# Optimization experiments

Measured on AMD Instinct MI355X. Metric: run time of the kernel, lower is better.

Reference implementation:

```python
import jax, jax.numpy as jnp
import numpy as np

B, F, H, OUT, S = 32768, 256, 128, 64, 6
RELAX, EPS, BN_EPS = 1.5, 1e-05, 1e-05
SQRT_HALF = 0.7071067811865476


def _bn(h, g, b):
    # training-mode BatchNorm1d: biased batch statistics over dim 0
    m = h.mean(axis=0)
    v = h.var(axis=0)
    return (h - m) * jax.lax.rsqrt(v + BN_EPS) * g + b


def _tfrm(x, W, g, b, glu_act=True):
    h = _bn(x @ W, g, b)
    if glu_act:
        d = h.shape[1] // 2
        h = h[:, :d] * jax.nn.sigmoid(h[:, d:])
    return h


def setup_inputs() -> dict:
    key = jax.random.key(0)
    ks = jax.random.split(key, 6)
    f32 = jnp.float32
    return {
        "x": jax.random.normal(ks[0], (B, F), f32),
        "enc_g": jnp.ones((F,), f32), "enc_b": jnp.zeros((F,), f32),
        "W1": jax.random.normal(ks[1], (F, 2 * H), f32) * 0.05,
        "g1": jnp.ones((2 * H,), f32), "b1": jnp.zeros((2 * H,), f32),
        "W2": jax.random.normal(ks[2], (H, 2 * H), f32) * 0.05,
        "g2": jnp.ones((2 * H,), f32), "b2": jnp.zeros((2 * H,), f32),
        "W3": jax.random.normal(ks[3], (S, H, 2 * H), f32) * 0.05,
        "g3": jnp.ones((S, 2 * H), f32), "b3": jnp.zeros((S, 2 * H), f32),
        "W4": jax.random.normal(ks[4], (S, H, 2 * H), f32) * 0.05,
        "g4": jnp.ones((S, 2 * H), f32), "b4": jnp.zeros((S, 2 * H), f32),
        "Wc": jax.random.normal(ks[5], (S - 1, OUT, F), f32) * 0.05,
        "gc": jnp.ones((S - 1, F), f32), "bc": jnp.zeros((S - 1, F), f32),
    }


def reference(x, enc_g, enc_b, W1, g1, b1, W2, g2, b2, W3, g3, b3,
              W4, g4, b4, Wc, gc, bc):
    x = _bn(x, enc_g, enc_b)                      # [B, F]
    masked = x
    compl = jnp.ones((x.shape[0], F), x.dtype)    # complementary aggregated mask
    agg_out, agg_entropy = [], []
    for ni in range(S):
        h = _tfrm(masked, W1, g1, b1)                             # [B, H]
        h = (_tfrm(h, W2, g2, b2) + h) * SQRT_HALF
        h = (_tfrm(h, W3[ni], g3[ni], b3[ni]) + h) * SQRT_HALF
        h = (_tfrm(h, W4[ni], g4[ni], b4[ni]) + h) * SQRT_HALF
        if ni > 0:
            # NOTE: source uses x (not h) here -- replicated faithfully
            agg_out.append(jax.nn.relu(x[:, :OUT]))
        fc = h[:, OUT:]                                           # [B, OUT]
        if ni < S - 1:
            coef = _tfrm(fc, Wc[ni], gc[ni], bc[ni], glu_act=False)  # [B, F]
            mask_values = jax.nn.softmax(coef * compl, axis=1)
            compl = compl * (RELAX - mask_values)
            agg_entropy.append(
                jnp.mean(jnp.sum(-mask_values * jnp.log(mask_values + EPS), axis=1))
                / (S - 1))
            masked = mask_values * x
    out = jnp.sum(jnp.stack(agg_out, axis=0), axis=0)   # [B, OUT]
    entropy = jnp.sum(jnp.stack(agg_entropy))           # scalar
    return (out, entropy)
```

## Files before the change

kernel.cpp:

```cpp
#include <hip/hip_runtime.h>
#include <math.h>

#define BSZ   32768
#define FDIM  256
#define HDIM  128
#define OUTD  64
#define SQRT_HALF 0.70710678118654752f
#define BN_EPS 1e-5f
#define SM_EPS 1e-5f
#define INV_B (1.0f / 32768.0f)
#define NCPY  8
#define SLOT  (NCPY * 512)

typedef __attribute__((ext_vector_type(8))) short bf16x8;
typedef __attribute__((ext_vector_type(4))) float f32x4;

__device__ __forceinline__ float b2f(unsigned short u) {
    return __uint_as_float(((unsigned int)u) << 16);
}
__device__ __forceinline__ unsigned short f2b(float f) {
    unsigned int u = __float_as_uint(f);
    u += 0x7fff + ((u >> 16) & 1);
    return (unsigned short)(u >> 16);
}

__device__ __forceinline__ void async16(const void* g, void* l) {
    __builtin_amdgcn_global_load_lds(
        (const __attribute__((address_space(1))) void*)(uintptr_t)g,
        (__attribute__((address_space(3))) void*)(unsigned int)(uintptr_t)l,
        16, 0, 0);
}

__device__ inline float waveMaxAll(float v) {
#pragma unroll
    for (int m = 32; m > 0; m >>= 1) v = fmaxf(v, __shfl_xor(v, m, 64));
    return v;
}
__device__ inline float waveSumAll(float v) {
#pragma unroll
    for (int m = 32; m > 0; m >>= 1) v += __shfl_xor(v, m, 64);
    return v;
}

__global__ __launch_bounds__(256) void prep_w(
    const float* __restrict__ W1, const float* __restrict__ W2,
    const float* __restrict__ W3, const float* __restrict__ W4,
    const float* __restrict__ Wc,
    unsigned short* __restrict__ W1t, unsigned short* __restrict__ W2t,
    unsigned short* __restrict__ W3t, unsigned short* __restrict__ W4t,
    unsigned short* __restrict__ Wct)
{
    const int m = blockIdx.x, kz = blockIdx.y, n = threadIdx.x;
    const float* src; unsigned short* dst; int K;
    if (m == 0)      { src = W1;                        dst = W1t;               K = 256; }
    else if (m == 1) { src = W2;                        dst = W2t;               K = 128; }
    else if (m < 7)  { int i = m - 2;  src = W3 + (size_t)i * 128 * 256; dst = W3t + (size_t)i * 32768; K = 128; }
    else if (m < 12) { int i = m - 7;  src = W4 + (size_t)i * 128 * 256; dst = W4t + (size_t)i * 32768; K = 128; }
    else             { int i = m - 12; src = Wc + (size_t)i * 64 * 256;  dst = Wct + (size_t)i * 16384; K = 64; }
    const int k0 = kz * 32;
    if (k0 >= K) return;
    for (int k = k0; k < k0 + 32; ++k)
        dst[(size_t)n * K + k] = f2b(src[(size_t)k * 256 + n]);
}

__global__ __launch_bounds__(256) void colstats(const float* __restrict__ X,
                                                float* __restrict__ st0) {
    __shared__ float red[4][512];
    const int sub = threadIdx.x >> 6;
    const int c4  = (threadIdx.x & 63) << 2;
    float s[4] = {0.f, 0.f, 0.f, 0.f}, q[4] = {0.f, 0.f, 0.f, 0.f};
#pragma unroll 8
    for (int i = 0; i < 32; ++i) {
        const int row = blockIdx.x * 128 + i * 4 + sub;
        float4 v = *(const float4*)(X + (size_t)row * 256 + c4);
        s[0] += v.x; q[0] += v.x * v.x;
        s[1] += v.y; q[1] += v.y * v.y;
        s[2] += v.z; q[2] += v.z * v.z;
        s[3] += v.w; q[3] += v.w * v.w;
    }
#pragma unroll
    for (int e = 0; e < 4; ++e) {
        red[sub][c4 + e] = s[e];
        red[sub][256 + c4 + e] = q[e];
    }
    __syncthreads();
    const int t = threadIdx.x;
    const int cp = (blockIdx.x & (NCPY - 1)) * 512;
    float sS = red[0][t] + red[1][t] + red[2][t] + red[3][t];
    float sQ = red[0][256 + t] + red[1][256 + t] + red[2][256 + t] + red[3][256 + t];
    atomicAdd(&st0[cp + t], sS);
    atomicAdd(&st0[cp + 256 + t], sQ);
}

__global__ __launch_bounds__(256) void norm_x(const float* __restrict__ x,
                                              const float* __restrict__ st0,
                                              const float* __restrict__ g,
                                              const float* __restrict__ b,
                                              unsigned short* __restrict__ xb,
                                              float* __restrict__ out) {
    const int i4 = blockIdx.x * 256 + threadIdx.x;
    const int row = i4 >> 6, c4 = (i4 & 63) << 2;
    float4 xv = *(const float4*)(x + (size_t)row * 256 + c4);
    float sS[4] = {0.f, 0.f, 0.f, 0.f}, sQ[4] = {0.f, 0.f, 0.f, 0.f};
#pragma unroll
    for (int cp = 0; cp < NCPY; ++cp) {
        float4 a = *(const float4*)&st0[cp * 512 + c4];
        float4 q = *(const float4*)&st0[cp * 512 + 256 + c4];
        sS[0] += a.x; sS[1] += a.y; sS[2] += a.z; sS[3] += a.w;
        sQ[0] += q.x; sQ[1] += q.y; sQ[2] += q.z; sQ[3] += q.w;
    }
    float4 gv = *(const float4*)&g[c4];
    float4 bv = *(const float4*)&b[c4];
    const float* xp = (const float*)&xv;
    const float* gp = (const float*)&gv; const float* bp = (const float*)&bv;
    float n[4];
    ushort4 ob;
    unsigned short* obp = (unsigned short*)&ob;
#pragma unroll
    for (int e = 0; e < 4; ++e) {
        float mean = sS[e] * INV_B;
        float var  = sQ[e] * INV_B - mean * mean;
        float sc   = gp[e] * rsqrtf(var + BN_EPS);
        float sh   = bp[e] - mean * sc;
        n[e] = xp[e] * sc + sh;
        obp[e] = f2b(n[e]);
    }
    *(ushort4*)(xb + (size_t)row * 256 + c4) = ob;
    if (c4 < OUTD) {
        float4 ov = make_float4(5.0f * fmaxf(n[0], 0.f), 5.0f * fmaxf(n[1], 0.f),
                                5.0f * fmaxf(n[2], 0.f), 5.0f * fmaxf(n[3], 0.f));
        *(float4*)(out + (size_t)row * OUTD + c4) = ov;
    }
}

__device__ __forceinline__ void gemm_epilogue(
    f32x4 (&acc)[4][4], int row0, int wave, int lane, int tid, int bcp,
    float* redS, float* redQ,
    unsigned short* __restrict__ Pout, float* __restrict__ statsOut)
{
    const int fm = lane & 15;
    const int orow = row0 + (lane >> 4) * 4;
    const int ocol = wave * 64 + fm;
#pragma unroll
    for (int i = 0; i < 4; ++i)
#pragma unroll
        for (int j = 0; j < 4; ++j)
#pragma unroll
            for (int r = 0; r < 4; ++r)
                Pout[(size_t)(orow + i * 16 + r) * 256 + (ocol + j * 16)] = f2b(acc[i][j][r]);

#pragma unroll
    for (int j = 0; j < 4; ++j) {
        float s = 0.f, q = 0.f;
#pragma unroll
        for (int i = 0; i < 4; ++i)
#pragma unroll
            for (int r = 0; r < 4; ++r) {
                float v = acc[i][j][r];
                s += v; q += v * v;
            }
        s += __shfl_xor(s, 16, 64); s += __shfl_xor(s, 32, 64);
        q += __shfl_xor(q, 16, 64); q += __shfl_xor(q, 32, 64);
        if (lane < 16) {
            redS[wave * 64 + j * 16 + lane] = s;
            redQ[wave * 64 + j * 16 + lane] = q;
        }
    }
    __syncthreads();
    atomicAdd(&statsOut[bcp + tid], redS[tid]);
    atomicAdd(&statsOut[bcp + 256 + tid], redQ[tid]);
}

__global__ __launch_bounds__(256) void gemm_bf16(
    const unsigned short* __restrict__ A,
    const unsigned short* __restrict__ Wt, int K,
    unsigned short* __restrict__ P,
    float* __restrict__ statsOut)
{
    __shared__ short As[64 * 32];
    __shared__ short Bs[256 * 32];
    __shared__ float redS[256], redQ[256];

    const int tid  = threadIdx.x;
    const int wave = tid >> 6;
    const int lane = tid & 63;
    const int row0 = blockIdx.x * 64;
    const int bcp  = (blockIdx.x & (NCPY - 1)) * 512;

    const int sr = lane >> 2;
    const int sc = (lane & 3) * 8;
    const int fm = lane & 15;
    const int fq = (lane >> 4) * 8;

    f32x4 acc[4][4];
#pragma unroll
    for (int i = 0; i < 4; ++i)
#pragma unroll
        for (int j = 0; j < 4; ++j)
            acc[i][j] = (f32x4){0.f, 0.f, 0.f, 0.f};

    for (int k0 = 0; k0 < K; k0 += 32) {
        async16(A + (size_t)(row0 + wave * 16 + sr) * K + k0 + sc,
                (void*)(As + wave * 512 + lane * 8));
#pragma unroll
        for (int t = 0; t < 4; ++t) {
            const int wr = wave * 64 + t * 16 + sr;
            async16(Wt + (size_t)wr * K + k0 + sc,
                    (void*)(Bs + (wave * 4 + t) * 512 + lane * 8));
        }
        __syncthreads();

        bf16x8 af[4], bfr[4];
#pragma unroll
        for (int i = 0; i < 4; ++i)
            af[i] = *(const bf16x8*)(As + (i * 16 + fm) * 32 + fq);
#pragma unroll
        for (int j = 0; j < 4; ++j)
            bfr[j] = *(const bf16x8*)(Bs + (wave * 64 + j * 16 + fm) * 32 + fq);
#pragma unroll
        for (int i = 0; i < 4; ++i)
#pragma unroll
            for (int j = 0; j < 4; ++j)
                acc[i][j] = __builtin_amdgcn_mfma_f32_16x16x32_bf16(af[i], bfr[j], acc[i][j], 0, 0, 0);
        __syncthreads();
    }

    gemm_epilogue(acc, row0, wave, lane, tid, bcp, redS, redQ, P, statsOut);
}

template <bool RES, bool WRITE_H>
__global__ __launch_bounds__(256) void gemm_glu(
    const unsigned short* __restrict__ Pprev,
    const float* __restrict__ pstats,
    const float* __restrict__ pg,
    const float* __restrict__ pb,
    const unsigned short* __restrict__ res,
    int colOff,
    const unsigned short* __restrict__ Wt, int K,
    unsigned short* __restrict__ Pout,
    float* __restrict__ statsOut,
    unsigned short* __restrict__ hOut)
{
    __shared__ short As[64 * 32];
    __shared__ short Bs[256 * 32];
    __shared__ float redS[256], redQ[256];
    __shared__ float tScA[128], tShA[128], tScG[128], tShG[128];

    const int tid  = threadIdx.x;
    const int wave = tid >> 6;
    const int lane = tid & 63;
    const int row0 = blockIdx.x * 64;
    const int bcp  = (blockIdx.x & (NCPY - 1)) * 512;

    if (tid < K) {
        const int ch = colOff + tid;
        const int cg = ch + 128;
        float sA = 0.f, qA = 0.f, sG = 0.f, qG = 0.f;
#pragma unroll
        for (int cp = 0; cp < NCPY; ++cp) {
            const float* p = pstats + cp * 512;
            sA += p[ch]; qA += p[256 + ch];
            sG += p[cg]; qG += p[256 + cg];
        }
        float ma = sA * INV_B, va = qA * INV_B - ma * ma;
        float scA = pg[ch] * rsqrtf(va + BN_EPS);
        tScA[tid] = scA; tShA[tid] = pb[ch] - ma * scA;
        float mg = sG * INV_B, vg = qG * INV_B - mg * mg;
        float scG = pg[cg] * rsqrtf(vg + BN_EPS);
        tScG[tid] = scG; tShG[tid] = pb[cg] - mg * scG;
    }
    __syncthreads();

    const int sr = lane >> 2;
    const int sc = (lane & 3) * 8;
    const int ar = tid >> 2;
    const int ac = (tid & 3) * 8;
    const int fm = lane & 15;
    const int fq = (lane >> 4) * 8;

    f32x4 acc[4][4];
#pragma unroll
    for (int i = 0; i < 4; ++i)
#pragma unroll
        for (int j = 0; j < 4; ++j)
            acc[i][j] = (f32x4){0.f, 0.f, 0.f, 0.f};

    for (int k0 = 0; k0 < K; k0 += 32) {
#pragma unroll
        for (int t = 0; t < 4; ++t) {
            const int wr = wave * 64 + t * 16 + sr;
            async16(Wt + (size_t)wr * K + k0 + sc,
                    (void*)(Bs + (wave * 4 + t) * 512 + lane * 8));
        }

        {
            const int kk = k0 + ac;
            const size_t grow = (size_t)(row0 + ar);

            bf16x8 lo = *(const bf16x8*)(Pprev + grow * 256 + colOff + kk);
            bf16x8 hi = *(const bf16x8*)(Pprev + grow * 256 + colOff + kk + 128);
            bf16x8 rv;
            if (RES) rv = *(const bf16x8*)(res + grow * 128 + kk);

            float4 a0 = *(const float4*)&tScA[kk], a1 = *(const float4*)&tScA[kk + 4];
            float4 h0 = *(const float4*)&tShA[kk], h1 = *(const float4*)&tShA[kk + 4];
            float4 g0 = *(const float4*)&tScG[kk], g1 = *(const float4*)&tScG[kk + 4];
            float4 s0 = *(const float4*)&tShG[kk], s1 = *(const float4*)&tShG[kk + 4];
            float scA[8] = {a0.x, a0.y, a0.z, a0.w, a1.x, a1.y, a1.z, a1.w};
            float shA[8] = {h0.x, h0.y, h0.z, h0.w, h1.x, h1.y, h1.z, h1.w};
            float scG[8] = {g0.x, g0.y, g0.z, g0.w, g1.x, g1.y, g1.z, g1.w};
            float shG[8] = {s0.x, s0.y, s0.z, s0.w, s1.x, s1.y, s1.z, s1.w};

            bf16x8 o8;
#pragma unroll
            for (int e = 0; e < 8; ++e) {
                float na = b2f((unsigned short)lo[e]) * scA[e] + shA[e];
                float ng = b2f((unsigned short)hi[e]) * scG[e] + shG[e];
                float v = na * (1.0f / (1.0f + __expf(-ng)));
                if (RES) v = (v + b2f((unsigned short)rv[e])) * SQRT_HALF;
                o8[e] = (short)f2b(v);
            }
            *(bf16x8*)(As + ar * 32 + ac) = o8;
            if (WRITE_H)
                *(bf16x8*)(hOut + grow * 128 + kk) = o8;
        }
        __syncthreads();

        bf16x8 af[4], bfr[4];
#pragma unroll
        for (int i = 0; i < 4; ++i)
            af[i] = *(const bf16x8*)(As + (i * 16 + fm) * 32 + fq);
#pragma unroll
        for (int j = 0; j < 4; ++j)
            bfr[j] = *(const bf16x8*)(Bs + (wave * 64 + j * 16 + fm) * 32 + fq);
#pragma unroll
        for (int i = 0; i < 4; ++i)
#pragma unroll
            for (int j = 0; j < 4; ++j)
                acc[i][j] = __builtin_amdgcn_mfma_f32_16x16x32_bf16(af[i], bfr[j], acc[i][j], 0, 0, 0);
        __syncthreads();
    }

    gemm_epilogue(acc, row0, wave, lane, tid, bcp, redS, redQ, Pout, statsOut);
}

template <int MODE>
__global__ __launch_bounds__(256) void coef_mask(const unsigned short* __restrict__ Pc,
                                                 const float* __restrict__ stats,
                                                 const float* __restrict__ gc,
                                                 const float* __restrict__ bc,
                                                 const unsigned short* __restrict__ xb,
                                                 unsigned short* __restrict__ cmpl,
                                                 unsigned short* __restrict__ masked,
                                                 float* __restrict__ ent) {
    const int w    = threadIdx.x >> 6;
    const int lane = threadIdx.x & 63;
    const int row  = blockIdx.x * 4 + w;
    const int c    = lane << 2;
    __shared__ float went[4];

    float sS[4] = {0.f, 0.f, 0.f, 0.f}, sQ[4] = {0.f, 0.f, 0.f, 0.f};
#pragma unroll
    for (int cp = 0; cp < NCPY; ++cp) {
        float4 a = *(const float4*)&stats[cp * 512 + c];
        float4 q = *(const float4*)&stats[cp * 512 + 256 + c];
        sS[0] += a.x; sS[1] += a.y; sS[2] += a.z; sS[3] += a.w;
        sQ[0] += q.x; sQ[1] += q.y; sQ[2] += q.z; sQ[3] += q.w;
    }
    float4 gv = *(const float4*)&gc[c];
    float4 bv = *(const float4*)&bc[c];
    const float* gvv = (const float*)&gv; const float* bvv = (const float*)&bv;

    float scl[4], shf[4];
#pragma unroll
    for (int e = 0; e < 4; ++e) {
        float mean = sS[e] * INV_B, var = sQ[e] * INV_B - mean * mean;
        scl[e] = gvv[e] * rsqrtf(var + BN_EPS);
        shf[e] = bvv[e] - mean * scl[e];
    }

    const size_t idx = (size_t)row * 256 + c;
    ushort4 pu = *(const ushort4*)(Pc + idx);
    const unsigned short* puv = (const unsigned short*)&pu;

    float cl[4] = {1.f, 1.f, 1.f, 1.f};
    if (MODE != 0) {
        ushort4 cu = *(const ushort4*)(cmpl + idx);
        const unsigned short* cuv = (const unsigned short*)&cu;
#pragma unroll
        for (int e = 0; e < 4; ++e) cl[e] = b2f(cuv[e]);
    }

    float l[4];
#pragma unroll
    for (int e = 0; e < 4; ++e) l[e] = (b2f(puv[e]) * scl[e] + shf[e]) * cl[e];

    float mx = waveMaxAll(fmaxf(fmaxf(l[0], l[1]), fmaxf(l[2], l[3])));
    float e0 = __expf(l[0] - mx), e1 = __expf(l[1] - mx),
          e2 = __expf(l[2] - mx), e3 = __expf(l[3] - mx);
    float inv = 1.0f / waveSumAll(e0 + e1 + e2 + e3);

    float m[4] = {e0 * inv, e1 * inv, e2 * inv, e3 * inv};

    float et = -m[0] * __logf(m[0] + SM_EPS) - m[1] * __logf(m[1] + SM_EPS)
             - m[2] * __logf(m[2] + SM_EPS) - m[3] * __logf(m[3] + SM_EPS);
    et = waveSumAll(et);
    if (lane == 0) went[w] = et;
    __syncthreads();
    if (threadIdx.x == 0) {
        float v = went[0] + went[1] + went[2] + went[3];
        atomicAdd(&ent[(blockIdx.x & 255) << 5], v * (INV_B * 0.2f));
    }

    if (MODE != 2) {
        ushort4 xu = *(const ushort4*)(xb + idx);
        const unsigned short* xuv = (const unsigned short*)&xu;
        ushort4 co, mo;
        unsigned short* cop = (unsigned short*)&co;
        unsigned short* mop = (unsigned short*)&mo;
#pragma unroll
        for (int e = 0; e < 4; ++e) {
            cop[e] = f2b(cl[e] * (1.5f - m[e]));
            mop[e] = f2b(m[e] * b2f(xuv[e]));
        }
        *(ushort4*)&cmpl[idx]   = co;
        *(ushort4*)&masked[idx] = mo;
    }
}

__global__ __launch_bounds__(64) void write_ent(const float* __restrict__ ent,
                                                float* __restrict__ dst) {
    const int lane = threadIdx.x;
    float v = 0.f;
#pragma unroll
    for (int i = 0; i < 4; ++i) v += ent[(lane + 64 * i) << 5];
    v = waveSumAll(v);
    if (lane == 0) dst[0] = v;
}

extern "C" void kernel_launch(void* const* d_in, const int* in_sizes, int n_in,
                              void* d_out, int out_size, void* d_ws, size_t ws_size,
                              hipStream_t stream) {
    const float* x     = (const float*)d_in[0];
    const float* enc_g = (const float*)d_in[1];
    const float* enc_b = (const float*)d_in[2];
    const float* W1 = (const float*)d_in[3];
    const float* g1 = (const float*)d_in[4];
    const float* b1 = (const float*)d_in[5];
    const float* W2 = (const float*)d_in[6];
    const float* g2 = (const float*)d_in[7];
    const float* b2 = (const float*)d_in[8];
    const float* W3 = (const float*)d_in[9];
    const float* g3 = (const float*)d_in[10];
    const float* b3 = (const float*)d_in[11];
    const float* W4 = (const float*)d_in[12];
    const float* g4 = (const float*)d_in[13];
    const float* b4 = (const float*)d_in[14];
    const float* Wc = (const float*)d_in[15];
    const float* gc = (const float*)d_in[16];
    const float* bc = (const float*)d_in[17];
    float* out = (float*)d_out;

    const size_t NBF = (size_t)BSZ * FDIM;
    const size_t NBH = (size_t)BSZ * HDIM;

    unsigned short* xb     = (unsigned short*)d_ws;
    unsigned short* masked = xb + NBF;
    unsigned short* Pb1    = masked + NBF;
    unsigned short* h1     = Pb1 + NBF;
    unsigned short* h2     = h1 + NBH;
    unsigned short* h3     = h2 + NBH;
    unsigned short* cmpl   = h3 + NBH;
    unsigned short* W1t    = cmpl + NBF;
    unsigned short* W2t    = W1t + 65536;
    unsigned short* W3t    = W2t + 32768;
    unsigned short* W4t    = W3t + 163840;
    unsigned short* Wct    = W4t + 163840;
    float* stats = (float*)(Wct + 81920);
    float* ent   = stats + 26 * SLOT;

    unsigned short* Pb2 = masked;

    hipMemsetAsync(stats, 0, (26 * SLOT + 256 * 32) * sizeof(float), stream);

    prep_w<<<dim3(17, 8), 256, 0, stream>>>(W1, W2, W3, W4, Wc, W1t, W2t, W3t, W4t, Wct);
    colstats<<<256, 256, 0, stream>>>(x, stats);
    norm_x<<<8192, 256, 0, stream>>>(x, stats, enc_g, enc_b, xb, out);

    for (int ni = 0; ni < 5; ++ni) {
        float* s1 = stats + (size_t)(1 + ni * 5 + 0) * SLOT;
        float* s2 = stats + (size_t)(1 + ni * 5 + 1) * SLOT;
        float* s3 = stats + (size_t)(1 + ni * 5 + 2) * SLOT;
        float* s4 = stats + (size_t)(1 + ni * 5 + 3) * SLOT;
        float* s5 = stats + (size_t)(1 + ni * 5 + 4) * SLOT;

        const unsigned short* in1 = (ni == 0) ? xb : masked;

        gemm_bf16<<<512, 256, 0, stream>>>(in1, W1t, 256, Pb1, s1);
        gemm_glu<false, true><<<512, 256, 0, stream>>>(
            Pb1, s1, g1, b1, nullptr, 0, W2t, 128, Pb2, s2, h1);
        gemm_glu<true, true><<<512, 256, 0, stream>>>(
            Pb2, s2, g2, b2, h1, 0, W3t + (size_t)ni * 32768, 128, Pb1, s3, h2);
        gemm_glu<true, true><<<512, 256, 0, stream>>>(
            Pb1, s3, g3 + ni * 256, b3 + ni * 256, h2, 0,
            W4t + (size_t)ni * 32768, 128, Pb2, s4, h3);
        gemm_glu<true, false><<<512, 256, 0, stream>>>(
            Pb2, s4, g4 + ni * 256, b4 + ni * 256, h3 + 64, 64,
            Wct + (size_t)ni * 16384, 64, Pb1, s5, nullptr);

        if (ni == 0)
            coef_mask<0><<<BSZ / 4, 256, 0, stream>>>(Pb1, s5, gc, bc, xb, cmpl, masked, ent);
        else if (ni < 4)
            coef_mask<1><<<BSZ / 4, 256, 0, stream>>>(Pb1, s5, gc + ni * 256, bc + ni * 256,
                                                      xb, cmpl, masked, ent);
        else
            coef_mask<2><<<BSZ / 4, 256, 0, stream>>>(Pb1, s5, gc + ni * 256, bc + ni * 256,
                                                      xb, cmpl, masked, ent);
    }

    write_ent<<<1, 64, 0, stream>>>(ent, out + (size_t)BSZ * OUTD);
}
```

Measured before the change: 612.2 us.

## Fuse coefficient softmax mask into the next step's first GEMM

The separate coef_mask kernel is folded into a new gemm_mask kernel. It computes the BN-normalised coefficients, softmax, entropy and complementary-mask update per 64-row tile, then writes the masked input into swizzled shared memory and runs the first layer's GEMM directly from it. This removes the global write and re-read of the masked activation and one launch per step. The cost is 32KB of extra LDS per block and 64 float registers per thread, which may reduce occupancy. Pc and Pout alias, which looks safe since each block reads only its own rows before writing them. The last step's entropy now goes through a separate coef_ent kernel.

```diff
diff --git a/kernel.cpp b/kernel.cpp
--- a/kernel.cpp
+++ b/kernel.cpp
@@ -228,6 +228,163 @@
     gemm_epilogue(acc, row0, wave, lane, tid, bcp, redS, redQ, P, statsOut);
 }
 
+template <int MODE>
+__global__ __launch_bounds__(256) void gemm_mask(
+    const unsigned short* Pc,
+    const float* __restrict__ cstats,
+    const float* __restrict__ gc, const float* __restrict__ bc,
+    const unsigned short* __restrict__ xb,
+    unsigned short* __restrict__ cmpl,
+    float* __restrict__ ent,
+    const unsigned short* __restrict__ Wt,
+    unsigned short* Pout,
+    float* __restrict__ statsOut)
+{
+    __shared__ short Am[64 * 256];
+    __shared__ short Bs[256 * 32];
+    __shared__ float redS[256], redQ[256];
+    __shared__ float tScl[256], tShf[256];
+    __shared__ float went[4];
+
+    const int tid  = threadIdx.x;
+    const int wave = tid >> 6;
+    const int lane = tid & 63;
+    const int row0 = blockIdx.x * 64;
+    const int bcp  = (blockIdx.x & (NCPY - 1)) * 512;
+
+    const int sr = lane >> 2;
+    const int sc = (lane & 3) * 8;
+
+#pragma unroll
+    for (int t = 0; t < 4; ++t) {
+        const int wr = wave * 64 + t * 16 + sr;
+        async16(Wt + (size_t)wr * 256 + sc,
+                (void*)(Bs + (wave * 4 + t) * 512 + lane * 8));
+    }
+
+    {
+        float s = 0.f, q = 0.f;
+#pragma unroll
+        for (int cp = 0; cp < NCPY; ++cp) {
+            s += cstats[cp * 512 + tid];
+            q += cstats[cp * 512 + 256 + tid];
+        }
+        float mean = s * INV_B, var = q * INV_B - mean * mean;
+        float scl_ = gc[tid] * rsqrtf(var + BN_EPS);
+        tScl[tid] = scl_;
+        tShf[tid] = bc[tid] - mean * scl_;
+    }
+    __syncthreads();
+
+    const int r = tid >> 2;
+    const int q4 = tid & 3;
+    const size_t grow = (size_t)(row0 + r) * 256;
+
+    float l[64];
+    float mx = -1e30f;
+#pragma unroll
+    for (int e = 0; e < 8; ++e) {
+        const int c = q4 * 64 + e * 8;
+        bf16x8 pv = *(const bf16x8*)(Pc + grow + c);
+        bf16x8 cv;
+        if (MODE) cv = *(const bf16x8*)(cmpl + grow + c);
+        float4 s0 = *(const float4*)&tScl[c], s1 = *(const float4*)&tScl[c + 4];
+        float4 h0 = *(const float4*)&tShf[c], h1 = *(const float4*)&tShf[c + 4];
+        const float* sp0 = (const float*)&s0; const float* sp1 = (const float*)&s1;
+        const float* hp0 = (const float*)&h0; const float* hp1 = (const float*)&h1;
+#pragma unroll
+        for (int t = 0; t < 8; ++t) {
+            float scl_ = (t < 4) ? sp0[t] : sp1[t - 4];
+            float shf_ = (t < 4) ? hp0[t] : hp1[t - 4];
+            float cl = MODE ? b2f((unsigned short)cv[t]) : 1.0f;
+            float v = (b2f((unsigned short)pv[t]) * scl_ + shf_) * cl;
+            l[e * 8 + t] = v;
+            mx = fmaxf(mx, v);
+        }
+    }
+    mx = fmaxf(mx, __shfl_xor(mx, 1, 64));
+    mx = fmaxf(mx, __shfl_xor(mx, 2, 64));
+
+    float ssum = 0.f;
+#pragma unroll
+    for (int i = 0; i < 64; ++i) { l[i] = __expf(l[i] - mx); ssum += l[i]; }
+    ssum += __shfl_xor(ssum, 1, 64);
+    ssum += __shfl_xor(ssum, 2, 64);
+    const float inv = 1.0f / ssum;
+
+    float et = 0.f;
+#pragma unroll
+    for (int e = 0; e < 8; ++e) {
+        const int c = q4 * 64 + e * 8;
+        bf16x8 xv = *(const bf16x8*)(xb + grow + c);
+        bf16x8 cv2;
+        if (MODE) cv2 = *(const bf16x8*)(cmpl + grow + c);
+        bf16x8 mo, co;
+#pragma unroll
+        for (int t = 0; t < 8; ++t) {
+            float m = l[e * 8 + t] * inv;
+            et -= m * __logf(m + SM_EPS);
+            float cl = MODE ? b2f((unsigned short)cv2[t]) : 1.0f;
+            co[t] = (short)f2b(cl * (1.5f - m));
+            mo[t] = (short)f2b(m * b2f((unsigned short)xv[t]));
+        }
+        *(bf16x8*)(cmpl + grow + c) = co;
+        unsigned int byte = (unsigned int)(r * 512 + c * 2);
+        byte ^= ((unsigned int)(r & 7)) << 4;
+        *(bf16x8*)((char*)Am + byte) = mo;
+    }
+    et += __shfl_xor(et, 1, 64);
+    et += __shfl_xor(et, 2, 64);
+    float wet = waveSumAll(et) * 0.25f;
+    if (lane == 0) went[wave] = wet;
+    __syncthreads();
+    if (tid == 0) {
+        float v = went[0] + went[1] + went[2] + went[3];
+        atomicAdd(&ent[(blockIdx.x & 255) << 5], v * (INV_B * 0.2f));
+    }
+
+    const int fm = lane & 15;
+    const int fq = (lane >> 4) * 8;
+
+    f32x4 acc[4][4];
+#pragma unroll
+    for (int i = 0; i < 4; ++i)
+#pragma unroll
+        for (int j = 0; j < 4; ++j)
+            acc[i][j] = (f32x4){0.f, 0.f, 0.f, 0.f};
+
+    for (int k0 = 0; k0 < 256; k0 += 32) {
+        bf16x8 af[4], bfr[4];
+#pragma unroll
+        for (int i = 0; i < 4; ++i) {
+            const int row = i * 16 + fm;
+            unsigned int byte = (unsigned int)(row * 512 + (k0 + fq) * 2);
+            byte ^= ((unsigned int)(row & 7)) << 4;
+            af[i] = *(const bf16x8*)((const char*)Am + byte);
+        }
+#pragma unroll
+        for (int j = 0; j < 4; ++j)
+            bfr[j] = *(const bf16x8*)(Bs + (wave * 64 + j * 16 + fm) * 32 + fq);
+#pragma unroll
+        for (int i = 0; i < 4; ++i)
+#pragma unroll
+            for (int j = 0; j < 4; ++j)
+                acc[i][j] = __builtin_amdgcn_mfma_f32_16x16x32_bf16(af[i], bfr[j], acc[i][j], 0, 0, 0);
+        __syncthreads();
+        if (k0 + 32 < 256) {
+#pragma unroll
+            for (int t = 0; t < 4; ++t) {
+                const int wr = wave * 64 + t * 16 + sr;
+                async16(Wt + (size_t)wr * 256 + (k0 + 32) + sc,
+                        (void*)(Bs + (wave * 4 + t) * 512 + lane * 8));
+            }
+            __syncthreads();
+        }
+    }
+
+    gemm_epilogue(acc, row0, wave, lane, tid, bcp, redS, redQ, Pout, statsOut);
+}
+
 template <bool RES, bool WRITE_H>
 __global__ __launch_bounds__(256) void gemm_glu(
     const unsigned short* __restrict__ Pprev,
@@ -344,15 +501,12 @@
     gemm_epilogue(acc, row0, wave, lane, tid, bcp, redS, redQ, Pout, statsOut);
 }
 
-template <int MODE>
-__global__ __launch_bounds__(256) void coef_mask(const unsigned short* __restrict__ Pc,
-                                                 const float* __restrict__ stats,
-                                                 const float* __restrict__ gc,
-                                                 const float* __restrict__ bc,
-                                                 const unsigned short* __restrict__ xb,
-                                                 unsigned short* __restrict__ cmpl,
-                                                 unsigned short* __restrict__ masked,
-                                                 float* __restrict__ ent) {
+__global__ __launch_bounds__(256) void coef_ent(const unsigned short* __restrict__ Pc,
+                                                const float* __restrict__ stats,
+                                                const float* __restrict__ gc,
+                                                const float* __restrict__ bc,
+                                                const unsigned short* __restrict__ cmpl,
+                                                float* __restrict__ ent) {
     const int w    = threadIdx.x >> 6;
     const int lane = threadIdx.x & 63;
     const int row  = blockIdx.x * 4 + w;
@@ -382,18 +536,13 @@
     const size_t idx = (size_t)row * 256 + c;
     ushort4 pu = *(const ushort4*)(Pc + idx);
     const unsigned short* puv = (const unsigned short*)&pu;
-
-    float cl[4] = {1.f, 1.f, 1.f, 1.f};
-    if (MODE != 0) {
-        ushort4 cu = *(const ushort4*)(cmpl + idx);
-        const unsigned short* cuv = (const unsigned short*)&cu;
-#pragma unroll
-        for (int e = 0; e < 4; ++e) cl[e] = b2f(cuv[e]);
-    }
+    ushort4 cu = *(const ushort4*)(cmpl + idx);
+    const unsigned short* cuv = (const unsigned short*)&cu;
 
     float l[4];
 #pragma unroll
-    for (int e = 0; e < 4; ++e) l[e] = (b2f(puv[e]) * scl[e] + shf[e]) * cl[e];
+    for (int e = 0; e < 4; ++e)
+        l[e] = (b2f(puv[e]) * scl[e] + shf[e]) * b2f(cuv[e]);
 
     float mx = waveMaxAll(fmaxf(fmaxf(l[0], l[1]), fmaxf(l[2], l[3])));
     float e0 = __expf(l[0] - mx), e1 = __expf(l[1] - mx),
@@ -410,21 +559,6 @@
     if (threadIdx.x == 0) {
         float v = went[0] + went[1] + went[2] + went[3];
         atomicAdd(&ent[(blockIdx.x & 255) << 5], v * (INV_B * 0.2f));
-    }
-
-    if (MODE != 2) {
-        ushort4 xu = *(const ushort4*)(xb + idx);
-        const unsigned short* xuv = (const unsigned short*)&xu;
-        ushort4 co, mo;
-        unsigned short* cop = (unsigned short*)&co;
-        unsigned short* mop = (unsigned short*)&mo;
-#pragma unroll
-        for (int e = 0; e < 4; ++e) {
-            cop[e] = f2b(cl[e] * (1.5f - m[e]));
-            mop[e] = f2b(m[e] * b2f(xuv[e]));
-        }
-        *(ushort4*)&cmpl[idx]   = co;
-        *(ushort4*)&masked[idx] = mo;
     }
 }
 
@@ -494,9 +628,19 @@
         float* s4 = stats + (size_t)(1 + ni * 5 + 3) * SLOT;
         float* s5 = stats + (size_t)(1 + ni * 5 + 4) * SLOT;
 
-        const unsigned short* in1 = (ni == 0) ? xb : masked;
-
-        gemm_bf16<<<512, 256, 0, stream>>>(in1, W1t, 256, Pb1, s1);
+        if (ni == 0) {
+            gemm_bf16<<<512, 256, 0, stream>>>(xb, W1t, 256, Pb1, s1);
+        } else {
+            float* s5p = stats + (size_t)(1 + (ni - 1) * 5 + 4) * SLOT;
+            if (ni == 1)
+                gemm_mask<0><<<512, 256, 0, stream>>>(
+                    Pb1, s5p, gc, bc, xb, cmpl, ent, W1t, Pb1, s1);
+            else
+                gemm_mask<1><<<512, 256, 0, stream>>>(
+                    Pb1, s5p, gc + (ni - 1) * 256, bc + (ni - 1) * 256,
+                    xb, cmpl, ent, W1t, Pb1, s1);
+        }
+
         gemm_glu<false, true><<<512, 256, 0, stream>>>(
             Pb1, s1, g1, b1, nullptr, 0, W2t, 128, Pb2, s2, h1);
         gemm_glu<true, true><<<512, 256, 0, stream>>>(
@@ -507,16 +651,11 @@
         gemm_glu<true, false><<<512, 256, 0, stream>>>(
             Pb2, s4, g4 + ni * 256, b4 + ni * 256, h3 + 64, 64,
             Wct + (size_t)ni * 16384, 64, Pb1, s5, nullptr);
-
-        if (ni == 0)
-            coef_mask<0><<<BSZ / 4, 256, 0, stream>>>(Pb1, s5, gc, bc, xb, cmpl, masked, ent);
-        else if (ni < 4)
-            coef_mask<1><<<BSZ / 4, 256, 0, stream>>>(Pb1, s5, gc + ni * 256, bc + ni * 256,
-                                                      xb, cmpl, masked, ent);
-        else
-            coef_mask<2><<<BSZ / 4, 256, 0, stream>>>(Pb1, s5, gc + ni * 256, bc + ni * 256,
-                                                      xb, cmpl, masked, ent);
-    }
+    }
+
+    coef_ent<<<BSZ / 4, 256, 0, stream>>>(
+        Pb1, stats + (size_t)(1 + 4 * 5 + 4) * SLOT,
+        gc + 4 * 256, bc + 4 * 256, cmpl, ent);
 
     write_ent<<<1, 64, 0, stream>>>(ent, out + (size_t)BSZ * OUTD);
 }
```

Result: faster. 598.0 us (-2.3%).
